# Optimization experiments

Hardware: AMD Instinct MI355X
Metric: run time of the kernel (lower is better)

## Reference

```python
import jax, jax.numpy as jnp
import numpy as np

WS = 8
SHIFT = 4


def _cpb_constants(ws):
    rc = np.arange(-(ws - 1), ws, dtype=np.float32)
    gh, gw = np.meshgrid(rc, rc, indexing='ij')
    table = np.stack([gh, gw], axis=-1)[None]  # (1, 2ws-1, 2ws-1, 2)
    table = table / (ws - 1) * 8.0
    table = np.sign(table) * np.log2(np.abs(table) + 1.0) / np.log2(8.0)
    c = np.arange(ws)
    ch, cw = np.meshgrid(c, c, indexing='ij')
    flat = np.stack([ch.ravel(), cw.ravel()])  # (2, N)
    rel = (flat[:, :, None] - flat[:, None, :]).transpose(1, 2, 0).copy()
    rel[..., 0] += ws - 1
    rel[..., 1] += ws - 1
    rel[..., 0] *= 2 * ws - 1
    rpi = rel.sum(-1)  # (N, N) int
    return table.astype(np.float32), rpi


def _attn_mask(H, W, ws, s):
    # Faithful to source: middle slice is slice(-ws, +s) (empty for H>ws+s)
    img = np.zeros((H, W), np.float32)
    cnt = 0
    for hs in (slice(0, -ws), slice(-ws, s), slice(-s, None)):
        for wsl in (slice(0, -ws), slice(-ws, s), slice(-s, None)):
            img[hs, wsl] = cnt
            cnt += 1
    mw = img.reshape(H // ws, ws, W // ws, ws).transpose(0, 2, 1, 3).reshape(-1, ws * ws)
    am = mw[:, None, :] - mw[:, :, None]
    return np.where(am != 0, -100.0, 0.0).astype(np.float32)


def _dwconv(x, w):
    return jax.lax.conv_general_dilated(
        x, w, (1, 1), 'SAME',
        dimension_numbers=('NCHW', 'OIHW', 'NCHW'),
        feature_group_count=x.shape[1])


def _ln_nchw(x, g, b, eps=8e-8):
    m = x.mean(1, keepdims=True)
    v = jnp.square(x - m).mean(1, keepdims=True)
    return (x - m) / jnp.sqrt(v + eps) * g[None, :, None, None] + b[None, :, None, None]


def setup_inputs() -> dict:
    key = jax.random.key(0)
    ks = jax.random.split(key, 16)
    B, C, H, W = 16, 512, 64, 64
    nh = 16
    hid = 4 * C
    w = lambda k, s: (jax.random.normal(k, s, dtype=jnp.float32) * 0.02)
    return {
        'x': jax.random.normal(ks[0], (B, C, H, W), dtype=jnp.float32),
        'lpu_w': w(ks[1], (C, 1, 3, 3)),
        'qkv_w': w(ks[2], (3 * C, C)),
        'out_w': w(ks[3], (C, C)),
        'cpb_w1': w(ks[4], (512, 2)),
        'cpb_w2': w(ks[5], (nh, 512)),
        'logits_scale': jnp.full((nh, 1, 1), np.log(10.0), dtype=jnp.float32),
        'gamma1': jnp.ones((C,), jnp.float32),
        'beta1': jnp.zeros((C,), jnp.float32),
        'gamma2': jnp.ones((C,), jnp.float32),
        'beta2': jnp.zeros((C,), jnp.float32),
        'pw1_w': w(ks[6], (hid, C)),
        'dw_w': w(ks[7], (hid, 1, 3, 3)),
        'pw2_w': w(ks[8], (C, hid)),
        'sr_scale': jnp.ones((), jnp.float32),
        'sr_bias': jnp.zeros((), jnp.float32),
        'rs1': jnp.ones((C,), jnp.float32),
        'rs2': jnp.ones((C,), jnp.float32),
    }


def reference(x, lpu_w, qkv_w, out_w, cpb_w1, cpb_w2, logits_scale,
              gamma1, beta1, gamma2, beta2, pw1_w, dw_w, pw2_w,
              sr_scale, sr_bias, rs1, rs2):
    B, C, H, W = x.shape
    ws, s = WS, SHIFT
    nh = logits_scale.shape[0]
    hd = C // nh
    N = ws * ws
    table_np, rpi = _cpb_constants(ws)
    table = jnp.asarray(table_np)
    mask = jnp.asarray(_attn_mask(H, W, ws, s))  # (nW, N, N)

    # LPU: x + depthwise conv
    x = x + _dwconv(x, lpu_w)
    x_temp = x

    # flatten to (B, HW, C); faithful roll over dims (1,2) = tokens AND channels
    x = x.reshape(B, C, H * W).transpose(0, 2, 1)
    x = jnp.roll(x, (-s, -s), axis=(1, 2))
    # window partition
    x = x.reshape(B, H // ws, ws, W // ws, ws, C).transpose(0, 1, 3, 2, 4, 5).reshape(-1, N, C)
    Bw = x.shape[0]

    qkv = (x @ qkv_w.T).reshape(Bw, N, 3, nh, hd).transpose(2, 0, 3, 1, 4)
    q, k, v = qkv[0], qkv[1], qkv[2]
    qn = q / jnp.maximum(jnp.linalg.norm(q, axis=-1, keepdims=True), 1e-12)
    kn = k / jnp.maximum(jnp.linalg.norm(k, axis=-1, keepdims=True), 1e-12)
    scale = jnp.exp(jnp.minimum(logits_scale, jnp.log(jnp.float32(100.0))))
    attn = jnp.einsum('bhid,bhjd->bhij', qn, kn) * scale[None]

    # continuous position bias
    tbl = jax.nn.hard_swish(table @ cpb_w1.T) @ cpb_w2.T  # (1, 2ws-1, 2ws-1, nh)
    tbl = tbl.reshape(-1, nh)
    bias = tbl[rpi.reshape(-1)].reshape(N, N, nh).transpose(2, 0, 1)
    bias = 16.0 * jax.nn.sigmoid(bias)
    attn = attn + bias[None]

    nW = mask.shape[0]
    attn = (attn.reshape(Bw // nW, nW, nh, N, N) + mask[None, :, None]).reshape(-1, nh, N, N)
    # faithful: nn.Softmax(1) -> softmax over HEAD axis
    attn = jax.nn.softmax(attn, axis=1)

    o = jnp.einsum('bhij,bhjd->bhid', attn, v).transpose(0, 2, 1, 3).reshape(Bw, N, C)
    o = o @ out_w.T

    o = o.reshape(B, H // ws, ws, W // ws, ws, C)
    o = jnp.roll(o, (s, s), axis=(1, 2))  # faithful: rolls window-grid / row dims
    # faithful buggy un-partition: transpose(1,2) then reshape
    o = o.transpose(0, 2, 1, 3, 4, 5).reshape(B, C, H, W)

    x = rs1[None, :, None, None] * x_temp + _ln_nchw(o, gamma1, beta1)

    h = jnp.einsum('bchw,oc->bohw', x, pw1_w)
    h = h + _dwconv(h, dw_w)
    h = sr_scale * jnp.square(jax.nn.relu(h)) + sr_bias  # StarReLU
    y = jnp.einsum('bchw,oc->bohw', h, pw2_w)
    return rs2[None, :, None, None] * x + _ln_nchw(y, gamma2, beta2)
```

## Files before the change

kernel.cpp:

```cpp
#include <hip/hip_runtime.h>
#include <hip/hip_bf16.h>
#include <stdint.h>


typedef float f32x4 __attribute__((ext_vector_type(4)));
typedef short s16x8 __attribute__((ext_vector_type(8)));

__device__ __forceinline__ float b2f(short u) {
  return __uint_as_float(((unsigned)(unsigned short)u) << 16);
}
__device__ __forceinline__ short f2b(float f) {
  unsigned x = __float_as_uint(f);
  unsigned r = (x + 0x7fffu + ((x >> 16) & 1u)) >> 16;
  return (short)r;
}
__device__ __forceinline__ void gload16(const void* g, void* l) {
  __builtin_amdgcn_global_load_lds((const unsigned int*)g, (unsigned int*)l, 16, 0, 0);
}

__global__ __launch_bounds__(256) void k_f2b(const float* __restrict__ s,
                                             short* __restrict__ d, int n) {
  int i = blockIdx.x * 256 + threadIdx.x;
  if (i < n) d[i] = f2b(s[i]);
}

__global__ __launch_bounds__(64) void k_cpb(const float* __restrict__ w1,
                                            const float* __restrict__ w2,
                                            float* __restrict__ btab) {
  const int r = blockIdx.x;
  const int lane = threadIdx.x;
  const int ri = r / 15, rj = r % 15;
  float th = (float)(ri - 7) * (8.f / 7.f);
  float tw = (float)(rj - 7) * (8.f / 7.f);
  float gh = copysignf(log2f(fabsf(th) + 1.f) * (1.f / 3.f), th);
  float gw = copysignf(log2f(fabsf(tw) + 1.f) * (1.f / 3.f), tw);
  const int h = lane >> 2, pp = lane & 3;
  float acc = 0.f;
  for (int k = 0; k < 128; ++k) {
    int hh = pp * 128 + k;
    float a = gh * w1[hh * 2] + gw * w1[hh * 2 + 1];
    float r6 = fminf(fmaxf(a + 3.f, 0.f), 6.f);
    float hsw = a * r6 * (1.f / 6.f);
    acc += hsw * w2[h * 512 + hh];
  }
  acc += __shfl_xor(acc, 1);
  acc += __shfl_xor(acc, 2);
  if ((lane & 3) == 0) btab[h * 225 + r] = 16.f / (1.f + __expf(-acc));
}

__global__ __launch_bounds__(256) void k_lpu(const float* __restrict__ x,
                                             const float* __restrict__ lw,
                                             short* __restrict__ xt) {
  __shared__ float img[64 * 68];
  const int bc = blockIdx.x;
  const int c = bc & 511;
  const float* img_g = x + (size_t)bc * 4096;
  short* outp = xt + (size_t)bc * 4096;
  const int tid = threadIdx.x;
#pragma unroll
  for (int t = 0; t < 4; ++t) {
    int idx = t * 256 + tid;
    int h = idx >> 4, w4 = (idx & 15) * 4;
    f32x4 v = *(const f32x4*)&img_g[h * 64 + w4];
    *(f32x4*)&img[h * 68 + w4] = v;
  }
  float wreg[9];
#pragma unroll
  for (int t = 0; t < 9; ++t) wreg[t] = lw[c * 9 + t];
  __syncthreads();
  const int hb = tid >> 4, w0 = (tid & 15) * 4;
#pragma unroll
  for (int g = 0; g < 4; ++g) {
    int h = hb + g * 16;
    float row[3][6];
#pragma unroll
    for (int dr = 0; dr < 3; ++dr) {
      int hh = h - 1 + dr;
      if (hh < 0 || hh > 63) {
#pragma unroll
        for (int j = 0; j < 6; ++j) row[dr][j] = 0.f;
      } else {
        f32x4 m = *(const f32x4*)&img[hh * 68 + w0];
        row[dr][1] = m[0]; row[dr][2] = m[1]; row[dr][3] = m[2]; row[dr][4] = m[3];
        row[dr][0] = (w0 > 0) ? img[hh * 68 + w0 - 1] : 0.f;
        row[dr][5] = (w0 < 60) ? img[hh * 68 + w0 + 4] : 0.f;
      }
    }
    ushort4 o;
    unsigned short op[4];
#pragma unroll
    for (int p = 0; p < 4; ++p) {
      float acc = row[1][p + 1];
#pragma unroll
      for (int dr = 0; dr < 3; ++dr)
#pragma unroll
        for (int dc = 0; dc < 3; ++dc)
          acc += wreg[dr * 3 + dc] * row[dr][p + dc];
      op[p] = (unsigned short)f2b(acc);
    }
    o.x = op[0]; o.y = op[1]; o.z = op[2]; o.w = op[3];
    *(ushort4*)&outp[h * 64 + w0] = o;
  }
}

__global__ __launch_bounds__(256) void k_xpose(const short* __restrict__ xt,
                                               short* __restrict__ xw) {
  __shared__ short tile[64][132];
  const int tid = threadIdx.x;
  const int cq = blockIdx.x & 3;
  const int h = (blockIdx.x >> 2) & 63;
  const int b = blockIdx.x >> 8;
  const int c0 = cq * 128;
  for (int idx = tid; idx < 64 * 128; idx += 256) {
    int ww = idx & 63, cc = idx >> 6;
    int csrc = (c0 + cc + 4) & 511;
    tile[ww][cc] = xt[(((size_t)b * 512 + csrc) * 64 + h) * 64 + ww];
  }
  __syncthreads();
  for (int qd = tid; qd < 64 * 32; qd += 256) {
    int ws_ = qd >> 5, cqq = qd & 31, cc = cqq * 4;
    int t = (h * 64 + ws_ + 4092) & 4095;
    int hd = t >> 6, wd = t & 63;
    int tok = (b * 64 + (hd >> 3) * 8 + (wd >> 3)) * 64 + (hd & 7) * 8 + (wd & 7);
    ushort4 u = *(const ushort4*)&tile[ws_][cc];
    *(ushort4*)&xw[(size_t)tok * 512 + c0 + cc] = u;
  }
}

template <int EPI>
__global__ __launch_bounds__(256) void k_gemm(const short* __restrict__ A,
                                              const short* __restrict__ B,
                                              short* __restrict__ C,
                                              short* __restrict__ o4,
                                              const float* __restrict__ lsc,
                                              int N, int K, int gx) {
  __shared__ short smem[2 * 128 * 64];
  short* As = smem;
  short* Bs = smem + 128 * 64;
  const int nwg = gridDim.x;
  const int orig = blockIdx.x;
  const int wgid = (orig & 7) * (nwg >> 3) + (orig >> 3);
  const int bx = wgid % gx, by = wgid / gx;
  const int tid = threadIdx.x;
  const int lane = tid & 63, wid = tid >> 6;
  const int wm = wid >> 1, wn = wid & 1;
  const int m0 = by * 128, n0 = bx * 128;
  const f32x4 fz = {0.f, 0.f, 0.f, 0.f};
  f32x4 acc[4][4];
#pragma unroll
  for (int m = 0; m < 4; ++m)
#pragma unroll
    for (int n = 0; n < 4; ++n) acc[m][n] = fz;
  const int rst = lane >> 3;
  const int cst = (((lane & 7) ^ rst)) * 8;
  const int l15 = lane & 15, l4 = lane >> 4, l7 = lane & 7;
  for (int k0 = 0; k0 < K; k0 += 64) {
#pragma unroll
    for (int i = 0; i < 4; ++i) {
      int rb = i * 4 + wid;
      int r = rb * 8 + rst;
      gload16(A + (size_t)(m0 + r) * K + k0 + cst, As + rb * 512);
      gload16(B + (size_t)(n0 + r) * K + k0 + cst, Bs + rb * 512);
    }
    __syncthreads();
#pragma unroll
    for (int ks = 0; ks < 2; ++ks) {
      s16x8 af[4], bfr[4];
#pragma unroll
      for (int m = 0; m < 4; ++m) {
        int row = wm * 64 + m * 16 + l15;
        af[m] = *(const s16x8*)&As[row * 64 + (((ks * 4 + l4) ^ l7) * 8)];
      }
#pragma unroll
      for (int n = 0; n < 4; ++n) {
        int row = wn * 64 + n * 16 + l15;
        bfr[n] = *(const s16x8*)&Bs[row * 64 + (((ks * 4 + l4) ^ l7) * 8)];
      }
#pragma unroll
      for (int m = 0; m < 4; ++m)
#pragma unroll
        for (int n = 0; n < 4; ++n)
          acc[m][n] = __builtin_amdgcn_mfma_f32_16x16x32_bf16(af[m], bfr[n],
                                                              acc[m][n], 0, 0, 0);
    }
    __syncthreads();
  }
  if (EPI == 2 && n0 < 1024) {
    const int cb = n0 + wn * 64;
    const bool isq = cb < 512;
    float sc0 = 1.f, sc1 = 1.f;
    if (isq) {
      sc0 = __expf(fminf(lsc[cb >> 5], 4.605170185988092f));
      sc1 = __expf(fminf(lsc[(cb >> 5) + 1], 4.605170185988092f));
    }
    if (cb < 1024) {
#pragma unroll
      for (int m = 0; m < 4; ++m)
#pragma unroll
        for (int np = 0; np < 2; ++np)
#pragma unroll
          for (int r = 0; r < 4; ++r) {
            float s0 = acc[m][2 * np][r], s1 = acc[m][2 * np + 1][r];
            float ss = s0 * s0 + s1 * s1;
            ss += __shfl_xor(ss, 1);
            ss += __shfl_xor(ss, 2);
            ss += __shfl_xor(ss, 4);
            ss += __shfl_xor(ss, 8);
            float mul = (np ? sc1 : sc0) / fmaxf(sqrtf(ss), 1e-12f);
            acc[m][2 * np][r] = s0 * mul;
            acc[m][2 * np + 1][r] = s1 * mul;
          }
    }
  }
  short* ct = smem;
  const int colslot = tid & 15;
#pragma unroll
  for (int half = 0; half < 2; ++half) {
    __syncthreads();
    if (wm == half) {
#pragma unroll
      for (int m = 0; m < 4; ++m)
#pragma unroll
        for (int n = 0; n < 4; ++n)
#pragma unroll
          for (int r = 0; r < 4; ++r) {
            int lr = m * 16 + l4 * 4 + r;
            int lc = wn * 64 + n * 16 + l15;
            ct[lr * 136 + lc] = f2b(acc[m][n][r]);
          }
    }
    __syncthreads();
#pragma unroll
    for (int ps = 0; ps < 4; ++ps) {
      int lr = (tid >> 4) + ps * 16;
      s16x8 v = *(const s16x8*)&ct[lr * 136 + colslot * 8];
      int grow = m0 + half * 64 + lr;
      int gcol = n0 + colslot * 8;
      if (EPI != 1) {
        *(s16x8*)&C[(size_t)grow * N + gcol] = v;
      } else {
        int win = grow >> 6, nn = grow & 63;
        int b = win >> 6, whs = (win >> 3) & 7, wws = win & 7;
        int ih = nn >> 3, iw = nn & 7;
        int wh = (whs + 4) & 7, ww = (wws + 4) & 7;
        int cp = ww * 64 + wh * 8 + ih;
        int hp = iw * 8 + (gcol >> 6);
        int wp = gcol & 63;
        *(s16x8*)&o4[(((size_t)b * 512 + cp) * 64 + hp) * 64 + wp] = v;
      }
    }
  }
}

__global__ __launch_bounds__(256) void k_attn(const short* __restrict__ qkv,
                                              const float* __restrict__ btab_g,
                                              short* __restrict__ o_ws) {
  __shared__ float btab[3600];
  __shared__ short vts[2][2048];
  __shared__ short pts[4][1024];
  const int tid = threadIdx.x, lane = tid & 63, wid = tid >> 6;
  const int win = blockIdx.x;
  const int l15 = lane & 15, l4 = lane >> 4;
  const int qrow0 = wid * 16;
  for (int i = tid; i < 3600; i += 256) btab[i] = btab_g[i];
  int baddr[4][4];
#pragma unroll
  for (int n = 0; n < 4; ++n)
#pragma unroll
    for (int r = 0; r < 4; ++r) {
      int i_ = qrow0 + l4 * 4 + r, j_ = n * 16 + l15;
      int dih = (i_ >> 3) - (j_ >> 3) + 7;
      int diw = (i_ & 7) - (j_ & 7) + 7;
      baddr[n][r] = dih * 15 + diw;
    }
  __syncthreads();
  const short* base = qkv + (size_t)win * 64 * 1536;
  const f32x4 fz = {0.f, 0.f, 0.f, 0.f};
  f32x4 sump[4] = {fz, fz, fz, fz};
#pragma unroll 2
  for (int h = 0; h < 16; ++h) {
    s16x8 qf = *(const s16x8*)(base + (size_t)(qrow0 + l15) * 1536 + h * 32 + l4 * 8);
#pragma unroll
    for (int n = 0; n < 4; ++n) {
      s16x8 kf = *(const s16x8*)(base + (size_t)(n * 16 + l15) * 1536 + 512 + h * 32 + l4 * 8);
      f32x4 s = __builtin_amdgcn_mfma_f32_16x16x32_bf16(qf, kf, fz, 0, 0, 0);
#pragma unroll
      for (int r = 0; r < 4; ++r)
        sump[n][r] += __expf(s[r] + btab[h * 225 + baddr[n][r]]);
    }
  }
  f32x4 rden[4];
#pragma unroll
  for (int n = 0; n < 4; ++n)
#pragma unroll
    for (int r = 0; r < 4; ++r) rden[n][r] = 1.f / sump[n][r];
  char* pt = (char*)pts[wid];
  {
    int j = tid & 63, d0 = (tid >> 6) * 8;
    s16x8 vv = *(const s16x8*)(base + (size_t)j * 1536 + 1024 + d0);
#pragma unroll
    for (int jj = 0; jj < 8; ++jj) {
      int d = d0 + jj;
      *(short*)((char*)vts[0] + ((d * 128 + j * 2) ^ ((d & 7) << 4))) = vv[jj];
    }
  }
  __syncthreads();
  for (int h = 0; h < 16; ++h) {
    const char* vcur = (const char*)vts[h & 1];
    if (h < 15) {
      int j = tid & 63, d0 = (tid >> 6) * 8;
      s16x8 vv = *(const s16x8*)(base + (size_t)j * 1536 + 1024 + (h + 1) * 32 + d0);
      char* vnxt = (char*)vts[(h + 1) & 1];
#pragma unroll
      for (int jj = 0; jj < 8; ++jj) {
        int d = d0 + jj;
        *(short*)(vnxt + ((d * 128 + j * 2) ^ ((d & 7) << 4))) = vv[jj];
      }
    }
    s16x8 qf = *(const s16x8*)(base + (size_t)(qrow0 + l15) * 1536 + h * 32 + l4 * 8);
#pragma unroll
    for (int n = 0; n < 4; ++n) {
      s16x8 kf = *(const s16x8*)(base + (size_t)(n * 16 + l15) * 1536 + 512 + h * 32 + l4 * 8);
      f32x4 s = __builtin_amdgcn_mfma_f32_16x16x32_bf16(qf, kf, fz, 0, 0, 0);
#pragma unroll
      for (int r = 0; r < 4; ++r) {
        float pv = __expf(s[r] + btab[h * 225 + baddr[n][r]]) * rden[n][r];
        int i_loc = l4 * 4 + r, j_ = n * 16 + l15;
        *(short*)(pt + ((i_loc * 128 + j_ * 2) ^ ((i_loc & 7) << 4))) = f2b(pv);
      }
    }
    f32x4 oacc[2] = {fz, fz};
#pragma unroll
    for (int kb = 0; kb < 2; ++kb) {
      s16x8 af = *(const s16x8*)(pt + ((l15 * 128 + kb * 64 + l4 * 16) ^ ((l15 & 7) << 4)));
#pragma unroll
      for (int db = 0; db < 2; ++db) {
        int d = db * 16 + l15;
        s16x8 bf = *(const s16x8*)(vcur + ((d * 128 + kb * 64 + l4 * 16) ^ ((d & 7) << 4)));
        oacc[db] = __builtin_amdgcn_mfma_f32_16x16x32_bf16(af, bf, oacc[db], 0, 0, 0);
      }
    }
    short* ob = o_ws + ((size_t)win * 64 + qrow0) * 512 + h * 32;
#pragma unroll
    for (int db = 0; db < 2; ++db)
#pragma unroll
      for (int r = 0; r < 4; ++r)
        ob[(size_t)(l4 * 4 + r) * 512 + db * 16 + l15] = f2b(oacc[db][r]);
    __syncthreads();
  }
}

__global__ __launch_bounds__(256) void k_ln1(const short* __restrict__ o4,
                                             const short* __restrict__ xt,
                                             const float* __restrict__ g1,
                                             const float* __restrict__ b1,
                                             const float* __restrict__ rs1,
                                             float* __restrict__ x2,
                                             short* __restrict__ x2h) {
  __shared__ float reds[4][64], redq[4][64];
  __shared__ float mean_s[64], rstd_s[64];
  __shared__ short tile[128][66];
  const int tid = threadIdx.x;
  const int b = blockIdx.x >> 6, hp = blockIdx.x & 63;
  const int w = tid & 63, part = tid >> 6;
  const short* base = o4 + (size_t)b * 512 * 4096 + hp * 64;
  float s = 0.f, q = 0.f;
  for (int c = part; c < 512; c += 4) {
    float v = b2f(base[(size_t)c * 4096 + w]);
    s += v; q += v * v;
  }
  reds[part][w] = s; redq[part][w] = q;
  __syncthreads();
  if (tid < 64) {
    float S = 0.f, Q = 0.f;
    for (int i = 0; i < 4; ++i) { S += reds[i][tid]; Q += redq[i][tid]; }
    float m = S * (1.f / 512.f);
    float var = Q * (1.f / 512.f) - m * m;
    mean_s[tid] = m;
    rstd_s[tid] = rsqrtf(var + 8e-8f);
  }
  __syncthreads();
  const short* xtb = xt + (size_t)b * 512 * 4096 + hp * 64;
  float* x2b = x2 + (size_t)b * 512 * 4096 + hp * 64;
  for (int c0 = 0; c0 < 512; c0 += 128) {
    for (int cc = part; cc < 128; cc += 4) {
      int c = c0 + cc;
      float v = b2f(base[(size_t)c * 4096 + w]);
      float ln = (v - mean_s[w]) * rstd_s[w] * g1[c] + b1[c];
      float xv = rs1[c] * b2f(xtb[(size_t)c * 4096 + w]) + ln;
      x2b[(size_t)c * 4096 + w] = xv;
      tile[cc][w] = f2b(xv);
    }
    __syncthreads();
    short* xh = x2h + ((size_t)blockIdx.x * 64) * 512 + c0;
    for (int qd = tid; qd < 64 * 32; qd += 256) {
      int w_ = qd >> 5, cq = qd & 31, cc = cq * 4;
      ushort4 u;
      u.x = (unsigned short)tile[cc][w_];
      u.y = (unsigned short)tile[cc + 1][w_];
      u.z = (unsigned short)tile[cc + 2][w_];
      u.w = (unsigned short)tile[cc + 3][w_];
      *(ushort4*)&xh[(size_t)w_ * 512 + cc] = u;
    }
    __syncthreads();
  }
}

__global__ __launch_bounds__(256) void k_dwc2(const short* __restrict__ h1,
                                              const float* __restrict__ dw,
                                              const float* __restrict__ srs_p,
                                              const float* __restrict__ srb_p,
                                              short* __restrict__ h2) {
  __shared__ short tile[6 * 64 * 64];
  const int tid = threadIdx.x;
  const int cblk = blockIdx.x & 31;
  const int hq = (blockIdx.x >> 5) & 15;
  const int b = blockIdx.x >> 9;
  const int c0 = cblk * 64;
  const int h0 = hq * 4;
  for (int t = 0; t < 12; ++t) {
    int idx = t * 256 + tid;
    int cg = idx & 7;
    int wl = (idx >> 3) & 63;
    int rl = idx >> 9;
    int hr = h0 - 1 + rl;
    s16x8 v = {0, 0, 0, 0, 0, 0, 0, 0};
    if (hr >= 0 && hr < 64)
      v = *(const s16x8*)&h1[((size_t)b * 4096 + hr * 64 + wl) * 2048 + c0 + cg * 8];
    *(s16x8*)&tile[(rl * 64 + wl) * 64 + (cg ^ (wl & 7)) * 8] = v;
  }
  const int cg = tid & 7;
  const int wq = tid >> 3;
  float wt[9][8];
#pragma unroll
  for (int j = 0; j < 8; ++j) {
    int cch = c0 + cg * 8 + j;
#pragma unroll
    for (int t = 0; t < 9; ++t) wt[t][j] = dw[cch * 9 + t];
  }
  const float srs = *srs_p, srb = *srb_p;
  __syncthreads();
#pragma unroll
  for (int it = 0; it < 8; ++it) {
    int wl = wq + (it & 1) * 32;
    int rl = it >> 1;
    s16x8 ctr = *(const s16x8*)&tile[((rl + 1) * 64 + wl) * 64 + (cg ^ (wl & 7)) * 8];
    float acc[8];
#pragma unroll
    for (int j = 0; j < 8; ++j) acc[j] = b2f(ctr[j]);
#pragma unroll
    for (int dh = -1; dh <= 1; ++dh) {
      int row = rl + 1 + dh;
#pragma unroll
      for (int dwi = -1; dwi <= 1; ++dwi) {
        int wn = wl + dwi;
        if (wn < 0 || wn > 63) continue;
        s16x8 v = *(const s16x8*)&tile[(row * 64 + wn) * 64 + (cg ^ (wn & 7)) * 8];
        const float* wrow = wt[(dh + 1) * 3 + dwi + 1];
#pragma unroll
        for (int j = 0; j < 8; ++j) acc[j] += wrow[j] * b2f(v[j]);
      }
    }
    s16x8 o;
#pragma unroll
    for (int j = 0; j < 8; ++j) {
      float rr = fmaxf(acc[j], 0.f);
      o[j] = f2b(srs * rr * rr + srb);
    }
    *(s16x8*)&h2[((size_t)b * 4096 + (h0 + rl) * 64 + wl) * 2048 + c0 + cg * 8] = o;
  }
}

__global__ __launch_bounds__(256) void k_final(const short* __restrict__ y,
                                               const float* __restrict__ x2,
                                               const float* __restrict__ g2,
                                               const float* __restrict__ b2p,
                                               const float* __restrict__ rs2,
                                               float* __restrict__ out) {
  __shared__ short yt[64][260];
  __shared__ float reds[4][64], redq[4][64];
  __shared__ float mean_s[64], rstd_s[64];
  const int tid = threadIdx.x;
  const int b = blockIdx.x >> 6, hh = blockIdx.x & 63;
  const int w = tid & 63, part = tid >> 6;
  const short* yb = y + (size_t)blockIdx.x * 64 * 512;
  float s = 0.f, q = 0.f;
  for (int c0 = 0; c0 < 512; c0 += 256) {
    __syncthreads();
    for (int qd = tid; qd < 64 * 64; qd += 256) {
      int w_ = qd >> 6, g = qd & 63;
      *(ushort4*)&yt[w_][g * 4] = *(const ushort4*)&yb[(size_t)w_ * 512 + c0 + g * 4];
    }
    __syncthreads();
    for (int cc = part * 64; cc < part * 64 + 64; ++cc) {
      float v = b2f(yt[w][cc]);
      s += v; q += v * v;
    }
  }
  reds[part][w] = s; redq[part][w] = q;
  __syncthreads();
  if (tid < 64) {
    float S = 0.f, Q = 0.f;
    for (int i = 0; i < 4; ++i) { S += reds[i][tid]; Q += redq[i][tid]; }
    float m = S * (1.f / 512.f);
    float var = Q * (1.f / 512.f) - m * m;
    mean_s[tid] = m;
    rstd_s[tid] = rsqrtf(var + 8e-8f);
  }
  __syncthreads();
  const float* x2b = x2 + (size_t)b * 512 * 4096 + hh * 64;
  float* ob = out + (size_t)b * 512 * 4096 + hh * 64;
  for (int pass = 0; pass < 2; ++pass) {
    int c0 = (pass == 0) ? 256 : 0;
    if (pass == 1) {
      __syncthreads();
      for (int qd = tid; qd < 64 * 64; qd += 256) {
        int w_ = qd >> 6, g = qd & 63;
        *(ushort4*)&yt[w_][g * 4] = *(const ushort4*)&yb[(size_t)w_ * 512 + g * 4];
      }
      __syncthreads();
    }
    for (int it = 0; it < 64; ++it) {
      int c = c0 + it * 4 + part;
      float yv = b2f(yt[w][c - c0]);
      float lnv = (yv - mean_s[w]) * rstd_s[w] * g2[c] + b2p[c];
      float xv = x2b[(size_t)c * 4096 + w];
      ob[(size_t)c * 4096 + w] = rs2[c] * xv + lnv;
    }
  }
}

extern "C" void kernel_launch(void* const* d_in, const int* in_sizes, int n_in,
                              void* d_out, int out_size, void* d_ws, size_t ws_size,
                              hipStream_t stream) {
  (void)in_sizes; (void)n_in; (void)out_size; (void)ws_size;
  const float* x      = (const float*)d_in[0];
  const float* lpu_w  = (const float*)d_in[1];
  const float* qkv_w  = (const float*)d_in[2];
  const float* out_w  = (const float*)d_in[3];
  const float* cpb_w1 = (const float*)d_in[4];
  const float* cpb_w2 = (const float*)d_in[5];
  const float* lsc    = (const float*)d_in[6];
  const float* g1     = (const float*)d_in[7];
  const float* b1     = (const float*)d_in[8];
  const float* g2     = (const float*)d_in[9];
  const float* b2v    = (const float*)d_in[10];
  const float* pw1_w  = (const float*)d_in[11];
  const float* dw_w   = (const float*)d_in[12];
  const float* pw2_w  = (const float*)d_in[13];
  const float* srs    = (const float*)d_in[14];
  const float* srb    = (const float*)d_in[15];
  const float* rs1    = (const float*)d_in[16];
  const float* rs2    = (const float*)d_in[17];

  char* ws = (char*)d_ws;
  float* btab   = (float*)(ws + 0);
  short* wbq    = (short*)(ws + 16384);
  short* wbo    = (short*)(ws + 1589248);
  short* wb1    = (short*)(ws + 2113536);
  short* wb2    = (short*)(ws + 4210688);
  short* x_temp = (short*)(ws + 8388608);
  short* xw     = (short*)(ws + 75497472);
  short* qkv    = (short*)(ws + 142606336);
  short* o_ws   = (short*)(ws + 343932928);
  short* o4     = (short*)(ws + 75497472);
  short* x2h    = (short*)(ws + 142606336);
  short* h1     = (short*)(ws + 209715200);
  short* h2     = (short*)(ws + 8388608);
  short* yb     = (short*)(ws + 343932928);
  float* x2     = (float*)d_out;

  k_f2b<<<3072, 256, 0, stream>>>(qkv_w, wbq, 786432);
  k_f2b<<<1024, 256, 0, stream>>>(out_w, wbo, 262144);
  k_f2b<<<4096, 256, 0, stream>>>(pw1_w, wb1, 1048576);
  k_f2b<<<4096, 256, 0, stream>>>(pw2_w, wb2, 1048576);
  k_cpb<<<225, 64, 0, stream>>>(cpb_w1, cpb_w2, btab);
  k_lpu<<<8192, 256, 0, stream>>>(x, lpu_w, x_temp);
  k_xpose<<<4096, 256, 0, stream>>>(x_temp, xw);
  k_gemm<2><<<6144, 256, 0, stream>>>(xw, wbq, qkv, nullptr, lsc, 1536, 512, 12);
  k_attn<<<1024, 256, 0, stream>>>(qkv, btab, o_ws);
  k_gemm<1><<<2048, 256, 0, stream>>>(o_ws, wbo, nullptr, o4, nullptr, 512, 512, 4);
  k_ln1<<<1024, 256, 0, stream>>>(o4, x_temp, g1, b1, rs1, x2, x2h);
  for (int ch = 0; ch < 2; ++ch) {
    const size_t tok0 = (size_t)ch * 8 * 4096;
    k_gemm<0><<<4096, 256, 0, stream>>>(x2h + tok0 * 512, wb1, h1, nullptr, nullptr, 2048, 512, 16);
    k_dwc2<<<4096, 256, 0, stream>>>(h1, dw_w, srs, srb, h2);
    k_gemm<0><<<1024, 256, 0, stream>>>(h2, wb2, yb + tok0 * 512, nullptr, nullptr, 512, 2048, 4);
  }
  k_final<<<1024, 256, 0, stream>>>(yb, x2, g2, b2v, rs2, (float*)d_out);
}
```

Baseline: 1.310 ms.

## Drop fp32 residual buffer, reuse bf16 x2h in final; single-pass GEMM epilogue

The LN1 kernel no longer writes the fp32 residual x2 into the output buffer. The final kernel instead reads the bf16 token-major copy x2h through a shared-memory tile, cutting a full fp32 write and reread of the activation tensor. The GEMM epilogue now stages the whole 128x128 tile in enlarged shared memory at once rather than in two halves, removing a pair of barriers. The residual path is now carried in bf16, which costs precision, and the larger LDS footprint may lower occupancy.

```diff
diff --git a/kernel.cpp b/kernel.cpp
--- a/kernel.cpp
+++ b/kernel.cpp
@@ -134,7 +134,7 @@
                                               short* __restrict__ o4,
                                               const float* __restrict__ lsc,
                                               int N, int K, int gx) {
-  __shared__ short smem[2 * 128 * 64];
+  __shared__ short smem[128 * 136];
   short* As = smem;
   short* Bs = smem + 128 * 64;
   const int nwg = gridDim.x;
@@ -187,13 +187,13 @@
   }
   if (EPI == 2 && n0 < 1024) {
     const int cb = n0 + wn * 64;
-    const bool isq = cb < 512;
-    float sc0 = 1.f, sc1 = 1.f;
-    if (isq) {
-      sc0 = __expf(fminf(lsc[cb >> 5], 4.605170185988092f));
-      sc1 = __expf(fminf(lsc[(cb >> 5) + 1], 4.605170185988092f));
-    }
     if (cb < 1024) {
+      const bool isq = cb < 512;
+      float sc0 = 1.f, sc1 = 1.f;
+      if (isq) {
+        sc0 = __expf(fminf(lsc[cb >> 5], 4.605170185988092f));
+        sc1 = __expf(fminf(lsc[(cb >> 5) + 1], 4.605170185988092f));
+      }
 #pragma unroll
       for (int m = 0; m < 4; ++m)
 #pragma unroll
@@ -213,41 +213,35 @@
     }
   }
   short* ct = smem;
+#pragma unroll
+  for (int m = 0; m < 4; ++m)
+#pragma unroll
+    for (int n = 0; n < 4; ++n)
+#pragma unroll
+      for (int r = 0; r < 4; ++r) {
+        int lr = wm * 64 + m * 16 + l4 * 4 + r;
+        int lc = wn * 64 + n * 16 + l15;
+        ct[lr * 136 + lc] = f2b(acc[m][n][r]);
+      }
+  __syncthreads();
   const int colslot = tid & 15;
 #pragma unroll
-  for (int half = 0; half < 2; ++half) {
-    __syncthreads();
-    if (wm == half) {
-#pragma unroll
-      for (int m = 0; m < 4; ++m)
-#pragma unroll
-        for (int n = 0; n < 4; ++n)
-#pragma unroll
-          for (int r = 0; r < 4; ++r) {
-            int lr = m * 16 + l4 * 4 + r;
-            int lc = wn * 64 + n * 16 + l15;
-            ct[lr * 136 + lc] = f2b(acc[m][n][r]);
-          }
-    }
-    __syncthreads();
-#pragma unroll
-    for (int ps = 0; ps < 4; ++ps) {
-      int lr = (tid >> 4) + ps * 16;
-      s16x8 v = *(const s16x8*)&ct[lr * 136 + colslot * 8];
-      int grow = m0 + half * 64 + lr;
-      int gcol = n0 + colslot * 8;
-      if (EPI != 1) {
-        *(s16x8*)&C[(size_t)grow * N + gcol] = v;
-      } else {
-        int win = grow >> 6, nn = grow & 63;
-        int b = win >> 6, whs = (win >> 3) & 7, wws = win & 7;
-        int ih = nn >> 3, iw = nn & 7;
-        int wh = (whs + 4) & 7, ww = (wws + 4) & 7;
-        int cp = ww * 64 + wh * 8 + ih;
-        int hp = iw * 8 + (gcol >> 6);
-        int wp = gcol & 63;
-        *(s16x8*)&o4[(((size_t)b * 512 + cp) * 64 + hp) * 64 + wp] = v;
-      }
+  for (int ps = 0; ps < 8; ++ps) {
+    int lr = (tid >> 4) + ps * 16;
+    s16x8 v = *(const s16x8*)&ct[lr * 136 + colslot * 8];
+    int grow = m0 + lr;
+    int gcol = n0 + colslot * 8;
+    if (EPI != 1) {
+      *(s16x8*)&C[(size_t)grow * N + gcol] = v;
+    } else {
+      int win = grow >> 6, nn = grow & 63;
+      int b = win >> 6, whs = (win >> 3) & 7, wws = win & 7;
+      int ih = nn >> 3, iw = nn & 7;
+      int wh = (whs + 4) & 7, ww = (wws + 4) & 7;
+      int cp = ww * 64 + wh * 8 + ih;
+      int hp = iw * 8 + (gcol >> 6);
+      int wp = gcol & 63;
+      *(s16x8*)&o4[(((size_t)b * 512 + cp) * 64 + hp) * 64 + wp] = v;
     }
   }
 }
@@ -355,7 +349,6 @@
                                              const float* __restrict__ g1,
                                              const float* __restrict__ b1,
                                              const float* __restrict__ rs1,
-                                             float* __restrict__ x2,
                                              short* __restrict__ x2h) {
   __shared__ float reds[4][64], redq[4][64];
   __shared__ float mean_s[64], rstd_s[64];
@@ -381,14 +374,12 @@
   }
   __syncthreads();
   const short* xtb = xt + (size_t)b * 512 * 4096 + hp * 64;
-  float* x2b = x2 + (size_t)b * 512 * 4096 + hp * 64;
   for (int c0 = 0; c0 < 512; c0 += 128) {
     for (int cc = part; cc < 128; cc += 4) {
       int c = c0 + cc;
       float v = b2f(base[(size_t)c * 4096 + w]);
       float ln = (v - mean_s[w]) * rstd_s[w] * g1[c] + b1[c];
       float xv = rs1[c] * b2f(xtb[(size_t)c * 4096 + w]) + ln;
-      x2b[(size_t)c * 4096 + w] = xv;
       tile[cc][w] = f2b(xv);
     }
     __syncthreads();
@@ -472,30 +463,32 @@
 }
 
 __global__ __launch_bounds__(256) void k_final(const short* __restrict__ y,
-                                               const float* __restrict__ x2,
+                                               const short* __restrict__ x2h,
                                                const float* __restrict__ g2,
                                                const float* __restrict__ b2p,
                                                const float* __restrict__ rs2,
                                                float* __restrict__ out) {
-  __shared__ short yt[64][260];
+  __shared__ short yt[64][132];
+  __shared__ short xt2[64][132];
   __shared__ float reds[4][64], redq[4][64];
   __shared__ float mean_s[64], rstd_s[64];
   const int tid = threadIdx.x;
   const int b = blockIdx.x >> 6, hh = blockIdx.x & 63;
   const int w = tid & 63, part = tid >> 6;
   const short* yb = y + (size_t)blockIdx.x * 64 * 512;
+  const short* xb = x2h + (size_t)blockIdx.x * 64 * 512;
   float s = 0.f, q = 0.f;
-  for (int c0 = 0; c0 < 512; c0 += 256) {
-    __syncthreads();
-    for (int qd = tid; qd < 64 * 64; qd += 256) {
-      int w_ = qd >> 6, g = qd & 63;
+  for (int c0 = 0; c0 < 512; c0 += 128) {
+    for (int qd = tid; qd < 64 * 32; qd += 256) {
+      int w_ = qd >> 5, g = qd & 31;
       *(ushort4*)&yt[w_][g * 4] = *(const ushort4*)&yb[(size_t)w_ * 512 + c0 + g * 4];
     }
     __syncthreads();
-    for (int cc = part * 64; cc < part * 64 + 64; ++cc) {
+    for (int cc = part * 32; cc < part * 32 + 32; ++cc) {
       float v = b2f(yt[w][cc]);
       s += v; q += v * v;
     }
+    __syncthreads();
   }
   reds[part][w] = s; redq[part][w] = q;
   __syncthreads();
@@ -508,25 +501,22 @@
     rstd_s[tid] = rsqrtf(var + 8e-8f);
   }
   __syncthreads();
-  const float* x2b = x2 + (size_t)b * 512 * 4096 + hh * 64;
   float* ob = out + (size_t)b * 512 * 4096 + hh * 64;
-  for (int pass = 0; pass < 2; ++pass) {
-    int c0 = (pass == 0) ? 256 : 0;
-    if (pass == 1) {
-      __syncthreads();
-      for (int qd = tid; qd < 64 * 64; qd += 256) {
-        int w_ = qd >> 6, g = qd & 63;
-        *(ushort4*)&yt[w_][g * 4] = *(const ushort4*)&yb[(size_t)w_ * 512 + g * 4];
-      }
-      __syncthreads();
-    }
-    for (int it = 0; it < 64; ++it) {
+  for (int c0 = 0; c0 < 512; c0 += 128) {
+    for (int qd = tid; qd < 64 * 32; qd += 256) {
+      int w_ = qd >> 5, g = qd & 31;
+      *(ushort4*)&yt[w_][g * 4] = *(const ushort4*)&yb[(size_t)w_ * 512 + c0 + g * 4];
+      *(ushort4*)&xt2[w_][g * 4] = *(const ushort4*)&xb[(size_t)w_ * 512 + c0 + g * 4];
+    }
+    __syncthreads();
+    for (int it = 0; it < 32; ++it) {
       int c = c0 + it * 4 + part;
       float yv = b2f(yt[w][c - c0]);
       float lnv = (yv - mean_s[w]) * rstd_s[w] * g2[c] + b2p[c];
-      float xv = x2b[(size_t)c * 4096 + w];
+      float xv = b2f(xt2[w][c - c0]);
       ob[(size_t)c * 4096 + w] = rs2[c] * xv + lnv;
     }
+    __syncthreads();
   }
 }
 
@@ -568,7 +558,6 @@
   short* h1     = (short*)(ws + 209715200);
   short* h2     = (short*)(ws + 8388608);
   short* yb     = (short*)(ws + 343932928);
-  float* x2     = (float*)d_out;
 
   k_f2b<<<3072, 256, 0, stream>>>(qkv_w, wbq, 786432);
   k_f2b<<<1024, 256, 0, stream>>>(out_w, wbo, 262144);
@@ -580,12 +569,12 @@
   k_gemm<2><<<6144, 256, 0, stream>>>(xw, wbq, qkv, nullptr, lsc, 1536, 512, 12);
   k_attn<<<1024, 256, 0, stream>>>(qkv, btab, o_ws);
   k_gemm<1><<<2048, 256, 0, stream>>>(o_ws, wbo, nullptr, o4, nullptr, 512, 512, 4);
-  k_ln1<<<1024, 256, 0, stream>>>(o4, x_temp, g1, b1, rs1, x2, x2h);
+  k_ln1<<<1024, 256, 0, stream>>>(o4, x_temp, g1, b1, rs1, x2h);
   for (int ch = 0; ch < 2; ++ch) {
     const size_t tok0 = (size_t)ch * 8 * 4096;
     k_gemm<0><<<4096, 256, 0, stream>>>(x2h + tok0 * 512, wb1, h1, nullptr, nullptr, 2048, 512, 16);
     k_dwc2<<<4096, 256, 0, stream>>>(h1, dw_w, srs, srb, h2);
     k_gemm<0><<<1024, 256, 0, stream>>>(h2, wb2, yb + tok0 * 512, nullptr, nullptr, 512, 2048, 4);
   }
-  k_final<<<1024, 256, 0, stream>>>(yb, x2, g2, b2v, rs2, (float*)d_out);
-}
+  k_final<<<1024, 256, 0, stream>>>(yb, x2h, g2, b2v, rs2, (float*)d_out);
+}
```

After: 1.223 ms. -6.7%, faster.
